# Optimization experiments

Hardware: AMD Instinct MI355X
Metric: run time of the kernel (lower is better)

Reference implementation:

```python
import jax, jax.numpy as jnp
import numpy as np

B, T, C = 2, 2048, 1024
H, DH = 16, 64  # num_heads, dim_head; inner_dim = H*DH = C


def setup_inputs() -> dict:
    key = jax.random.key(0)
    k_x, k_q, k_k, k_v, k_o, k_r = jax.random.split(key, 6)
    scaled = lambda k, shape, fan: (jax.random.normal(k, shape, jnp.float32) / np.sqrt(fan).astype(np.float32))
    x = jax.random.normal(k_x, (B, T, C), jnp.float32)
    Wq = scaled(k_q, (C, H * DH), C)
    Wk = scaled(k_k, (C, H * DH), C)
    Wv = scaled(k_v, (C, H * DH), C)
    Wo = scaled(k_o, (H * DH, C), H * DH)
    bo = jnp.zeros((C,), jnp.float32)
    # learned relative position bias table, indexed by (i - j) in [-(T-1), T-1]
    rel_table = jax.random.normal(k_r, (H, 2 * T - 1), jnp.float32) * 0.02
    # causal mask, broadcast over batch and heads
    mask = jnp.tril(jnp.ones((T, T), bool))[None, None]  # [1,1,T,T]
    return {"x": x, "Wq": Wq, "Wk": Wk, "Wv": Wv, "Wo": Wo, "bo": bo,
            "rel_table": rel_table, "mask": mask}


def reference(x, Wq, Wk, Wv, Wo, bo, rel_table, mask):
    Bx, Tx, Cx = x.shape
    split = lambda t: t.reshape(Bx, Tx, H, DH).transpose(0, 2, 1, 3)  # [B,H,T,DH]
    q = split(x @ Wq) * (DH ** -0.5)
    k = split(x @ Wk)
    v = split(x @ Wv)
    # relative position bias: bias[h,i,j] = rel_table[h, i-j + T-1]
    rel_idx = jnp.arange(Tx)[:, None] - jnp.arange(Tx)[None, :] + (Tx - 1)  # [T,T]
    bias = rel_table[:, rel_idx]  # [H,T,T]
    score = jnp.einsum('bhid,bhjd->bhij', q, k) + bias[None]
    mask_value = -jnp.finfo(score.dtype).max
    score = jnp.where(mask, score, mask_value)
    attn = jax.nn.softmax(score, axis=-1)
    y = jnp.einsum('bhij,bhjd->bhid', attn, v)
    y = y.transpose(0, 2, 1, 3).reshape(Bx, Tx, H * DH)
    return y @ Wo + bo
```

## Files before the change

kernel.cpp:

```cpp
#include <hip/hip_runtime.h>
#include <hip/hip_bf16.h>
#include <stdint.h>


#define T_SEQ 2048
#define NH    16
#define DHD   64
#define CDIM  1024

typedef unsigned short u16;
typedef unsigned int   u32;
typedef __attribute__((ext_vector_type(8))) __bf16 bf16x8;
typedef __attribute__((ext_vector_type(4))) float f32x4;

#define WAITL0   asm volatile("s_waitcnt lgkmcnt(0)" ::: "memory")

__device__ __forceinline__ float bf2f(u16 b){
  union { u32 u; float f; } v; v.u = ((u32)b) << 16; return v.f;
}
__device__ __forceinline__ u16 f2bf(float f){
  union { __bf16 h; u16 u; } v; v.h = (__bf16)f;
  return v.u;
}

__device__ __forceinline__ void gload_lds16(const u16* g, u16* l){
  __builtin_amdgcn_global_load_lds(
      (const __attribute__((address_space(1))) void*)g,
      (__attribute__((address_space(3))) void*)l, 16, 0, 0);
}

__device__ __forceinline__ uint4 load8(const void* p, long elem, int isbf){
  if (isbf) return *(const uint4*)((const u16*)p + elem);
  const float* fp = (const float*)p + elem;
  float4 a = *(const float4*)fp, b = *(const float4*)(fp + 4);
  uint4 r;
  r.x = (u32)f2bf(a.x) | ((u32)f2bf(a.y) << 16);
  r.y = (u32)f2bf(a.z) | ((u32)f2bf(a.w) << 16);
  r.z = (u32)f2bf(b.x) | ((u32)f2bf(b.y) << 16);
  r.w = (u32)f2bf(b.z) | ((u32)f2bf(b.w) << 16);
  return r;
}
__device__ __forceinline__ float loadf(const void* p, long idx, int isbf){
  return isbf ? bf2f(((const u16*)p)[idx]) : ((const float*)p)[idx];
}

__global__ __launch_bounds__(256) void classify(const u32* __restrict__ x,
                                                int* __restrict__ flag){
  __shared__ int cnt[256];
  int c = 0;
#pragma unroll
  for (int i = 0; i < 16; i++){
    u32 w = x[threadIdx.x * 16 + i];
    int e = (w >> 7) & 0xFF;
    c += (e >= 110 && e <= 140);
  }
  cnt[threadIdx.x] = c;
  __syncthreads();
  for (int s = 128; s > 0; s >>= 1){
    if ((int)threadIdx.x < s) cnt[threadIdx.x] += cnt[threadIdx.x + s];
    __syncthreads();
  }
  if (threadIdx.x == 0) *flag = (cnt[0] > 2048) ? 1 : 0;
}

__global__ __launch_bounds__(256) void cvt_x(const void* __restrict__ x,
                                             u16* __restrict__ xbf,
                                             const int* __restrict__ flag){
  const int isbf = *flag;
  const long i = ((long)blockIdx.x * 256 + threadIdx.x) * 8;
  *(uint4*)(xbf + i) = load8(x, i, isbf);
}

__global__ __launch_bounds__(256) void transposeW(
    const void* __restrict__ w0, const void* __restrict__ w1,
    const void* __restrict__ w2,
    u16* __restrict__ o0, u16* __restrict__ o1, u16* __restrict__ o2,
    const int* __restrict__ flag)
{
  __shared__ u16 tile[64][72];
  const int isbf = *flag;
  const int z = blockIdx.z;
  const void* in = z==0 ? w0 : z==1 ? w1 : w2;
  u16*      out  = z==0 ? o0 : z==1 ? o1 : o2;
  const int tid = threadIdx.x;
  const int r0 = blockIdx.y * 64, c0 = blockIdx.x * 64;
  const int rr = tid >> 3;
  const int cc = (tid & 7) * 8;
#pragma unroll
  for (int rd = 0; rd < 2; rd++){
    int r = rd*32 + rr;
    *(uint4*)&tile[r][cc] = load8(in, (long)(r0 + r)*CDIM + c0 + cc, isbf);
  }
  __syncthreads();
#pragma unroll
  for (int rd = 0; rd < 2; rd++){
    int oc = rd*32 + rr;
    uint4 wv; u32* wp = (u32*)&wv;
#pragma unroll
    for (int t = 0; t < 4; t++){
      u32 lo = tile[cc + 2*t][oc];
      u32 hi = tile[cc + 2*t + 1][oc];
      wp[t] = lo | (hi << 16);
    }
    *(uint4*)(out + (long)(c0 + oc)*CDIM + r0 + cc) = wv;
  }
}

__device__ __forceinline__ void gemm_body(
    const u16* __restrict__ A, const u16* __restrict__ BT,
    const void* __restrict__ bias, void* __restrict__ out,
    float scale, int mode, int m0, int n0, int io_isbf)
{
  __shared__ u16 ldsA[2][128*32];
  __shared__ u16 ldsB[2][128*32];
  const int tid = threadIdx.x;
  const int wid = tid >> 6, lane = tid & 63;
  const int col = lane & 15, quad = lane >> 4;
  const int wm = (wid >> 1) * 64, wn = (wid & 1) * 64;

  const int c0 = wid*128 + lane, c1 = c0 + 64;
  const int r0c = c0 >> 2, g0c = c0 & 3;
  const int r1c = c1 >> 2, g1c = c1 & 3;
  const long aoff0 = (long)r0c*CDIM + ((g0c ^ (r0c & 3)) << 3);
  const long aoff1 = (long)r1c*CDIM + ((g1c ^ (r1c & 3)) << 3);
  const int lds0 = (wid*128)*8;
  const int lds1 = (wid*128 + 64)*8;

  const u16* gA = A  + (long)m0*CDIM;
  const u16* gB = BT + (long)n0*CDIM;

  auto stage = [&](int buf, int k0){
    gload_lds16(gA + k0 + aoff0, &ldsA[buf][lds0]);
    gload_lds16(gA + k0 + aoff1, &ldsA[buf][lds1]);
    gload_lds16(gB + k0 + aoff0, &ldsB[buf][lds0]);
    gload_lds16(gB + k0 + aoff1, &ldsB[buf][lds1]);
  };

  f32x4 acc[4][4] = {};
  const int NK = CDIM / 32;

  stage(0, 0);
  __syncthreads();

  int cur = 0;
  for (int k = 0; k < NK; k++){
    if (k + 1 < NK) stage(cur ^ 1, (k + 1) * 32);

    bf16x8 af[4], bfr[4];
#pragma unroll
    for (int mi = 0; mi < 4; mi++){
      const int r = wm + mi*16 + col;
      af[mi] = *(const bf16x8*)&ldsA[cur][r*32 + ((quad ^ (r & 3)) * 8)];
    }
#pragma unroll
    for (int ni = 0; ni < 4; ni++){
      const int r = wn + ni*16 + col;
      bfr[ni] = *(const bf16x8*)&ldsB[cur][r*32 + ((quad ^ (r & 3)) * 8)];
    }
#pragma unroll
    for (int mi = 0; mi < 4; mi++)
#pragma unroll
      for (int ni = 0; ni < 4; ni++)
        acc[mi][ni] = __builtin_amdgcn_mfma_f32_16x16x32_bf16(af[mi], bfr[ni], acc[mi][ni], 0, 0, 0);

    __syncthreads();
    cur ^= 1;
  }

  if (mode == 2){
#pragma unroll
    for (int ni = 0; ni < 4; ni++){
      const int n = n0 + wn + ni*16 + col;
      const int h = n >> 6, d = n & 63;
#pragma unroll
      for (int mi = 0; mi < 4; mi++){
        const int m = m0 + wm + mi*16 + quad*4;
        const int b = m >> 11, t = m & (T_SEQ-1);
        uint2 pk;
        pk.x = (u32)f2bf(acc[mi][ni][0]) | ((u32)f2bf(acc[mi][ni][1]) << 16);
        pk.y = (u32)f2bf(acc[mi][ni][2]) | ((u32)f2bf(acc[mi][ni][3]) << 16);
        *(uint2*)((u16*)out + ((long)(b*NH + h)*DHD + d)*T_SEQ + t) = pk;
      }
    }
  } else {
#pragma unroll
    for (int ni = 0; ni < 4; ni++){
      const int n = n0 + wn + ni*16 + col;
      const float bv = bias ? loadf(bias, n, io_isbf) : 0.f;
#pragma unroll
      for (int mi = 0; mi < 4; mi++){
#pragma unroll
        for (int r = 0; r < 4; r++){
          const int m = m0 + wm + mi*16 + quad*4 + r;
          const float v = acc[mi][ni][r] * scale + bv;
          if (mode == 0){
            const long idx = (long)m*CDIM + n;
            if (io_isbf) ((u16*)out)[idx] = f2bf(v);
            else         ((float*)out)[idx] = v;
          } else {
            const int b = m >> 11, t = m & (T_SEQ-1), h = n >> 6, d = n & 63;
            ((u16*)out)[((long)(b*NH + h)*T_SEQ + t)*DHD + d] = f2bf(v);
          }
        }
      }
    }
  }
}

__global__ __launch_bounds__(256) void gemm_qkv(
    const u16* __restrict__ xbf,
    const u16* __restrict__ WqT, const u16* __restrict__ WkT, const u16* __restrict__ WvT,
    u16* __restrict__ Qb, u16* __restrict__ Kb, u16* __restrict__ VTb)
{
  const int z = blockIdx.z;
  const u16* BT = z==0 ? WqT : z==1 ? WkT : WvT;
  u16*      dst = z==0 ? Qb  : z==1 ? Kb  : VTb;
  const float scale = (z==0) ? 0.125f * 1.44269504f : 1.0f;
  const int mode = (z==2) ? 2 : 1;
  gemm_body(xbf, BT, nullptr, dst, scale, mode, blockIdx.x*128, blockIdx.y*128, 1);
}

__global__ __launch_bounds__(256) void gemm_out(
    const u16* __restrict__ Y, const u16* __restrict__ WoT,
    const void* __restrict__ bo, void* __restrict__ out,
    const int* __restrict__ flag)
{
  gemm_body(Y, WoT, bo, out, 1.0f, 0, blockIdx.x*128, blockIdx.y*128, *flag);
}

__global__ __launch_bounds__(256) void attn64(
    const u16* __restrict__ Q, const u16* __restrict__ K, const u16* __restrict__ VT,
    const void* __restrict__ rel, u16* __restrict__ Y,
    const int* __restrict__ flag)
{
  __shared__ u16 ldsK[2][64*64];
  __shared__ u16 ldsV[2][64*64];
  __shared__ u16 ldsP[4][16*88];
  __shared__ float ldsBias[2112];

  const int isbf = *flag;
  const int tid = threadIdx.x, wid = tid >> 6, lane = tid & 63;
  const int col = lane & 15, quad = lane >> 4;

  const int l = (int)blockIdx.x;
  const int xcd = l & 7, s = l >> 3;
  const int bh = xcd * 4 + (s & 3);
  const int g = s >> 2, gq = g >> 3, g0 = g & 7;
  const int ti = (gq == 0) ? 31 - g0
               : (gq == 1) ? g0
               : (gq == 2) ? 23 - g0
                           : 8 + g0;
  const int i0 = ti * 64;

  const int h = bh & (NH - 1);
  const int b = bh >> 4;

  const u16* Qh = Q  + (long)bh * T_SEQ * DHD;
  const u16* Kh = K  + (long)bh * T_SEQ * DHD;
  const u16* Vh = VT + (long)bh * DHD * T_SEQ;
  const long relbase = (long)h * (2*T_SEQ - 1) + (T_SEQ - 1);
  const float MLOG = 16.0f * 1.44269504f;

  const int srow0 = wid*8 + (lane >> 3);
  const int srow1 = srow0 + 32;
  const int soff  = ((lane & 7) ^ ((lane >> 3) & 7)) * 8;
  const int sb0   = wid*512;
  const int sb1   = 2048 + wid*512;

  auto stage = [&](int buf, int j0){
    gload_lds16(Kh + (long)(j0 + srow0)*DHD + soff, &ldsK[buf][sb0]);
    gload_lds16(Kh + (long)(j0 + srow1)*DHD + soff, &ldsK[buf][sb1]);
    gload_lds16(Vh + (long)srow0*T_SEQ + j0 + soff, &ldsV[buf][sb0]);
    gload_lds16(Vh + (long)srow1*T_SEQ + j0 + soff, &ldsV[buf][sb1]);
  };

  const int nbias = i0 + 127;
  for (int t = tid; t < nbias; t += 256)
    ldsBias[t] = loadf(rel, relbase + t - 63, isbf) * 1.44269504f - MLOG;

  bf16x8 qf0, qf1;
  {
    const u16* qp = Qh + (long)(i0 + wid*16 + col)*DHD + quad*8;
    qf0 = *(const bf16x8*)qp;
    qf1 = *(const bf16x8*)(qp + 32);
  }

  f32x4 O[4] = {};
  float lsumv = 0.f;
  const int icol = i0 + wid*16 + col;
  const int irow = i0 + wid*16 + quad*4;

  stage(0, 0);
  __syncthreads();

  int cur = 0;
  for (int j0 = 0; j0 <= i0; j0 += 64){
    const bool have_next = (j0 + 64 <= i0);
    if (have_next) stage(cur ^ 1, j0 + 64);

    f32x4 sv[4] = {};
#pragma unroll
    for (int kb = 0; kb < 2; kb++){
#pragma unroll
      for (int nb = 0; nb < 4; nb++){
        const int row = nb*16 + col;
        const int sl = ((kb*4 + quad) ^ (row & 7)) * 8;
        bf16x8 kf = *(const bf16x8*)&ldsK[cur][row*64 + sl];
        sv[nb] = __builtin_amdgcn_mfma_f32_16x16x32_bf16(kf, kb ? qf1 : qf0, sv[nb], 0, 0, 0);
      }
    }

    const bool diag = (j0 == i0);
#pragma unroll
    for (int nb = 0; nb < 4; nb++){
      const float* bp = &ldsBias[icol - j0 - nb*16 - quad*4 + 63];
#pragma unroll
      for (int r = 0; r < 4; r++){
        float arg = sv[nb][r] + bp[-r];
        if (diag && (nb*16 + quad*4 + r > wid*16 + col)) arg = -1e9f;
        float p;
        asm volatile("v_exp_f32 %0, %1" : "=v"(p) : "v"(arg));
        sv[nb][r] = p;
        lsumv += p;
      }
    }

    u16* Pw = ldsP[wid];
#pragma unroll
    for (int nb = 0; nb < 4; nb++){
      u32 lo, hi;
      asm("v_cvt_pk_bf16_f32 %0, %1, %2" : "=v"(lo) : "v"(sv[nb][0]), "v"(sv[nb][1]));
      asm("v_cvt_pk_bf16_f32 %0, %1, %2" : "=v"(hi) : "v"(sv[nb][2]), "v"(sv[nb][3]));
      uint2 pk; pk.x = lo; pk.y = hi;
      *(uint2*)&Pw[col*88 + nb*16 + quad*4] = pk;
    }
    WAITL0;

#pragma unroll
    for (int kb = 0; kb < 2; kb++){
      bf16x8 pf = *(const bf16x8*)&Pw[col*88 + kb*32 + quad*8];
#pragma unroll
      for (int nb = 0; nb < 4; nb++){
        const int row = nb*16 + col;
        const int sl = ((kb*4 + quad) ^ (row & 7)) * 8;
        bf16x8 vf = *(const bf16x8*)&ldsV[cur][row*64 + sl];
        O[nb] = __builtin_amdgcn_mfma_f32_16x16x32_bf16(pf, vf, O[nb], 0, 0, 0);
      }
    }

    __syncthreads();
    cur ^= 1;
  }

  lsumv += __shfl_xor(lsumv, 16, 64);
  lsumv += __shfl_xor(lsumv, 32, 64);
  float rs[4];
#pragma unroll
  for (int r = 0; r < 4; r++)
    rs[r] = __shfl(lsumv, quad*4 + r, 16);

#pragma unroll
  for (int nb = 0; nb < 4; nb++){
#pragma unroll
    for (int r = 0; r < 4; r++){
      const int i = irow + r;
      const int d = nb*16 + col;
      Y[((long)(b*T_SEQ + i))*CDIM + h*DHD + d] = f2bf(O[nb][r] / rs[r]);
    }
  }
}

extern "C" void kernel_launch(void* const* d_in, const int* in_sizes, int n_in,
                              void* d_out, int out_size, void* d_ws, size_t ws_size,
                              hipStream_t stream)
{
  (void)in_sizes; (void)n_in; (void)out_size; (void)ws_size;
  const void* x   = d_in[0];
  const void* Wq  = d_in[1];
  const void* Wk  = d_in[2];
  const void* Wv  = d_in[3];
  const void* Wo  = d_in[4];
  const void* bo  = d_in[5];
  const void* rel = d_in[6];

  char* ws = (char*)d_ws;
  const size_t MB = 1024*1024;
  int* flag = (int*)ws;
  char* base = ws + 256;
  u16* WqT = (u16*)(base + 0*MB);
  u16* WkT = (u16*)(base + 2*MB);
  u16* WvT = (u16*)(base + 4*MB);
  u16* Kb  = (u16*)(base + 6*MB);
  u16* VTb = (u16*)(base + 14*MB);
  u16* Yb  = (u16*)(base + 0*MB);
  u16* WoT = (u16*)(base + 8*MB);
  u16* Qb  = (u16*)d_out;
  u16* xbf = Qb + 4u*1024*1024;

  dim3 blk(256);
  classify  <<<1, blk, 0, stream>>>((const u32*)x, flag);
  cvt_x     <<<dim3(2048), blk, 0, stream>>>(x, xbf, flag);
  transposeW<<<dim3(16,16,3), blk, 0, stream>>>(Wq, Wk, Wv, WqT, WkT, WvT, flag);
  gemm_qkv  <<<dim3(32,8,3),  blk, 0, stream>>>(xbf, WqT, WkT, WvT, Qb, Kb, VTb);
  attn64    <<<dim3(1024),  blk, 0, stream>>>(Qb, Kb, VTb, rel, Yb, flag);
  transposeW<<<dim3(16,16,1), blk, 0, stream>>>(Wo, Wo, Wo, WoT, WoT, WoT, flag);
  gemm_out  <<<dim3(32,8),    blk, 0, stream>>>(Yb, WoT, bo, d_out, flag);
}
```

Baseline: 217.0 us.

## Keep softmax probabilities in registers and feed PV via 16x16x16 MFMA

Drops the per-wave LDS round trip for the probability tile. The QK^T accumulator layout is reused directly as the A operand of 16x16x16 bf16 MFMAs, with V fragments read as 4-element chunks to match. The bias table is stored as bf16 in LDS, halving its footprint, and the max-log offset is folded into the accumulator init. A launch-bounds occupancy hint of 4 is also added. The PV step now issues twice as many smaller MFMAs and more, smaller V loads, and the bias loses precision by being held in bf16.

```diff
diff --git a/kernel.cpp b/kernel.cpp
--- a/kernel.cpp
+++ b/kernel.cpp
@@ -11,9 +11,8 @@
 typedef unsigned short u16;
 typedef unsigned int   u32;
 typedef __attribute__((ext_vector_type(8))) __bf16 bf16x8;
+typedef __attribute__((ext_vector_type(4))) __bf16 bf16x4;
 typedef __attribute__((ext_vector_type(4))) float f32x4;
-
-#define WAITL0   asm volatile("s_waitcnt lgkmcnt(0)" ::: "memory")
 
 __device__ __forceinline__ float bf2f(u16 b){
   union { u32 u; float f; } v; v.u = ((u32)b) << 16; return v.f;
@@ -228,15 +227,14 @@
   gemm_body(Y, WoT, bo, out, 1.0f, 0, blockIdx.x*128, blockIdx.y*128, *flag);
 }
 
-__global__ __launch_bounds__(256) void attn64(
+__global__ __launch_bounds__(256, 4) void attn64(
     const u16* __restrict__ Q, const u16* __restrict__ K, const u16* __restrict__ VT,
     const void* __restrict__ rel, u16* __restrict__ Y,
     const int* __restrict__ flag)
 {
   __shared__ u16 ldsK[2][64*64];
   __shared__ u16 ldsV[2][64*64];
-  __shared__ u16 ldsP[4][16*88];
-  __shared__ float ldsBias[2112];
+  __shared__ u16 ldsBias[2112];
 
   const int isbf = *flag;
   const int tid = threadIdx.x, wid = tid >> 6, lane = tid & 63;
@@ -276,7 +274,7 @@
 
   const int nbias = i0 + 127;
   for (int t = tid; t < nbias; t += 256)
-    ldsBias[t] = loadf(rel, relbase + t - 63, isbf) * 1.44269504f - MLOG;
+    ldsBias[t] = f2bf(loadf(rel, relbase + t - 63, isbf) * 1.44269504f);
 
   bf16x8 qf0, qf1;
   {
@@ -289,6 +287,7 @@
   float lsumv = 0.f;
   const int icol = i0 + wid*16 + col;
   const int irow = i0 + wid*16 + quad*4;
+  const f32x4 minit = {-MLOG, -MLOG, -MLOG, -MLOG};
 
   stage(0, 0);
   __syncthreads();
@@ -298,7 +297,7 @@
     const bool have_next = (j0 + 64 <= i0);
     if (have_next) stage(cur ^ 1, j0 + 64);
 
-    f32x4 sv[4] = {};
+    f32x4 sv[4] = {minit, minit, minit, minit};
 #pragma unroll
     for (int kb = 0; kb < 2; kb++){
 #pragma unroll
@@ -313,10 +312,10 @@
     const bool diag = (j0 == i0);
 #pragma unroll
     for (int nb = 0; nb < 4; nb++){
-      const float* bp = &ldsBias[icol - j0 - nb*16 - quad*4 + 63];
+      const u16* bp = &ldsBias[icol - j0 - nb*16 - quad*4 + 63];
 #pragma unroll
       for (int r = 0; r < 4; r++){
-        float arg = sv[nb][r] + bp[-r];
+        float arg = sv[nb][r] + bf2f(bp[-r]);
         if (diag && (nb*16 + quad*4 + r > wid*16 + col)) arg = -1e9f;
         float p;
         asm volatile("v_exp_f32 %0, %1" : "=v"(p) : "v"(arg));
@@ -325,26 +324,27 @@
       }
     }
 
-    u16* Pw = ldsP[wid];
+    bf16x4 pa[4];
 #pragma unroll
     for (int nb = 0; nb < 4; nb++){
       u32 lo, hi;
       asm("v_cvt_pk_bf16_f32 %0, %1, %2" : "=v"(lo) : "v"(sv[nb][0]), "v"(sv[nb][1]));
       asm("v_cvt_pk_bf16_f32 %0, %1, %2" : "=v"(hi) : "v"(sv[nb][2]), "v"(sv[nb][3]));
       uint2 pk; pk.x = lo; pk.y = hi;
-      *(uint2*)&Pw[col*88 + nb*16 + quad*4] = pk;
-    }
-    WAITL0;
-
-#pragma unroll
-    for (int kb = 0; kb < 2; kb++){
-      bf16x8 pf = *(const bf16x8*)&Pw[col*88 + kb*32 + quad*8];
+      pa[nb] = *(bf16x4*)&pk;
+    }
+
+    const int vbase = (quad & 1) * 4;
+#pragma unroll
+    for (int jb = 0; jb < 4; jb++){
+      const int gch = jb*2 + (quad >> 1);
 #pragma unroll
       for (int nb = 0; nb < 4; nb++){
         const int row = nb*16 + col;
-        const int sl = ((kb*4 + quad) ^ (row & 7)) * 8;
-        bf16x8 vf = *(const bf16x8*)&ldsV[cur][row*64 + sl];
-        O[nb] = __builtin_amdgcn_mfma_f32_16x16x32_bf16(pf, vf, O[nb], 0, 0, 0);
+        const int off = row*64 + ((gch ^ (row & 7)) * 8) + vbase;
+        bf16x4 vf = *(const bf16x4*)&ldsV[cur][off];
+        asm("v_mfma_f32_16x16x16_bf16 %0, %1, %2, %0"
+            : "+v"(O[nb]) : "v"(pa[jb]), "v"(vf));
       }
     }
 
```

After: 222.3 us. +2.5%, slower.
